# Kernel optimization log

Measured on AMD Instinct MI355X. Metric: run time of the kernel, lower is better.

The kernel has to match this reference:

```python
import jax, jax.numpy as jnp
import numpy as np
from jax import lax

N_IMG = 2
LEVEL_HW = [(200, 200), (100, 100), (50, 50), (25, 25), (13, 13)]
STRIDES = [4, 8, 16, 32, 64]
SIZES = [32.0, 64.0, 128.0, 256.0, 512.0]
A = 3
LEVEL_SIZES = [A * h * w for h, w in LEVEL_HW]
R = sum(LEVEL_SIZES)  # 159882
PRE_NMS = 1000   # pre_nms_top_n['testing']
POST_NMS = 1000  # post_nms_top_n['testing']
NMS_THRESH = 0.7
SCORE_THRESH = 0.0
MIN_SIZE = 1e-3
IMG_H = IMG_W = 800.0
BBOX_XFORM_CLIP = float(np.log(1000.0 / 16.0))


def _make_anchors():
    ratios = np.array([0.5, 1.0, 2.0])
    h_r = np.sqrt(ratios)
    w_r = 1.0 / h_r
    out = []
    for (h, w), stride, size in zip(LEVEL_HW, STRIDES, SIZES):
        ws = size * w_r
        hs = size * h_r
        base = np.stack([-ws / 2, -hs / 2, ws / 2, hs / 2], 1)  # [A,4]
        sx = (np.arange(w) + 0.5) * stride
        sy = (np.arange(h) + 0.5) * stride
        yy, xx = np.meshgrid(sy, sx, indexing='ij')
        shifts = np.stack([xx.ravel(), yy.ravel(), xx.ravel(), yy.ravel()], 1)  # [H*W,4]
        out.append((shifts[:, None, :] + base[None, :, :]).reshape(-1, 4))
    return np.concatenate(out, 0).astype(np.float32)  # [R,4]


def setup_inputs() -> dict:
    key = jax.random.key(0)
    k1, k2 = jax.random.split(key)
    objectness = jax.random.normal(k1, (N_IMG, R), jnp.float32)
    deltas = jax.random.normal(k2, (N_IMG, R, 4), jnp.float32) * 0.2
    anchors = jnp.asarray(_make_anchors())
    return {"objectness": objectness, "deltas": deltas, "anchors": anchors}


def _decode(deltas, anchors):
    # BoxCoder.decode with weights (1,1,1,1)
    wa = anchors[:, 2] - anchors[:, 0]
    ha = anchors[:, 3] - anchors[:, 1]
    cxa = anchors[:, 0] + 0.5 * wa
    cya = anchors[:, 1] + 0.5 * ha
    dx, dy, dw, dh = deltas[..., 0], deltas[..., 1], deltas[..., 2], deltas[..., 3]
    dw = jnp.minimum(dw, BBOX_XFORM_CLIP)
    dh = jnp.minimum(dh, BBOX_XFORM_CLIP)
    cx = dx * wa + cxa
    cy = dy * ha + cya
    w = jnp.exp(dw) * wa
    h = jnp.exp(dh) * ha
    return jnp.stack([cx - 0.5 * w, cy - 0.5 * h, cx + 0.5 * w, cy + 0.5 * h], -1)


def _nms_single(boxes, scores, lvl, valid):
    # batched_nms via per-level coordinate offset trick
    offs = lvl.astype(boxes.dtype) * (max(IMG_H, IMG_W) + 1.0)
    ob = boxes + offs[:, None]
    s = jnp.where(valid, scores, -1.0)
    order = jnp.argsort(-s)
    b = ob[order]          # offset boxes, score-descending
    raw = boxes[order]     # original boxes
    v = valid[order]
    ss = s[order]
    area = (b[:, 2] - b[:, 0]) * (b[:, 3] - b[:, 1])
    lt = jnp.maximum(b[:, None, :2], b[None, :, :2])
    rb = jnp.minimum(b[:, None, 2:], b[None, :, 2:])
    wh = jnp.clip(rb - lt, 0.0)
    inter = wh[..., 0] * wh[..., 1]
    iou = inter / (area[:, None] + area[None, :] - inter + 1e-9)  # [K,K]
    K = b.shape[0]

    def body(keep, i):
        suppressed = jnp.any(keep & (iou[:, i] > NMS_THRESH))
        keep = keep.at[i].set(v[i] & ~suppressed)
        return keep, None

    keep, _ = lax.scan(body, jnp.zeros((K,), bool), jnp.arange(K))
    # compact kept boxes (score order preserved) into fixed POST_NMS slots
    pos = jnp.where(keep, jnp.minimum(jnp.cumsum(keep) - 1, POST_NMS), POST_NMS)
    out_b = jnp.zeros((POST_NMS + 1, 4), boxes.dtype).at[pos].set(raw)[:POST_NMS]
    out_s = jnp.full((POST_NMS + 1,), -1.0, boxes.dtype).at[pos].set(ss)[:POST_NMS]
    return out_b, out_s


def _forward(objectness, deltas, anchors):
    proposals = _decode(deltas, anchors)  # [N,R,4]
    # per-level topk (pre_nms_top_n)
    idxs = []
    off = 0
    for n in LEVEL_SIZES:
        k = min(PRE_NMS, n)
        _, ti = lax.top_k(objectness[:, off:off + n], k)
        idxs.append(ti + off)
        off += n
    top_idx = jnp.concatenate(idxs, 1)  # [N,K]
    obj = jnp.take_along_axis(objectness, top_idx, 1)
    boxes = jnp.take_along_axis(proposals, top_idx[..., None], 1)
    levels = jnp.concatenate([jnp.full((n,), i, jnp.int32) for i, n in enumerate(LEVEL_SIZES)])
    lvl = levels[top_idx]
    scores = jax.nn.sigmoid(obj)
    # clip_boxes_to_image
    x1 = jnp.clip(boxes[..., 0], 0.0, IMG_W)
    y1 = jnp.clip(boxes[..., 1], 0.0, IMG_H)
    x2 = jnp.clip(boxes[..., 2], 0.0, IMG_W)
    y2 = jnp.clip(boxes[..., 3], 0.0, IMG_H)
    boxes = jnp.stack([x1, y1, x2, y2], -1)
    # remove_small_boxes + score_thresh -> validity mask (fixed shapes)
    valid = (x2 - x1 >= MIN_SIZE) & (y2 - y1 >= MIN_SIZE) & (scores >= SCORE_THRESH)
    return jax.vmap(_nms_single)(boxes, scores, lvl, valid)


def reference(objectness, deltas, anchors):
    return _forward(objectness, deltas, anchors)
```

## Files before the change

kernel.cpp:

```cpp
#include <hip/hip_runtime.h>

typedef unsigned long long u64;
typedef unsigned int u32;

#define R_TOT 159882
#define POST 1000
#define IMG_SZ 800.0f
#define NMS_TH 0.7f
#define BBOX_CLIP 4.135166556742356f
#define LCAP 1024

__device__ __forceinline__ float fadd_(float a, float b){ return __fadd_rn(a,b); }
__device__ __forceinline__ float fsub_(float a, float b){ return __fsub_rn(a,b); }
__device__ __forceinline__ float fmul_(float a, float b){ return __fmul_rn(a,b); }

__device__ __forceinline__ int lvl_len(int l){ const int L[5]={120000,30000,7500,1875,507}; return L[l]; }
__device__ __forceinline__ int lvl_off(int l){ const int L[5]={0,120000,150000,157500,159375}; return L[l]; }
__device__ __forceinline__ int lvl_k(int l){ const int L[5]={1000,1000,1000,1000,507}; return L[l]; }

__device__ __forceinline__ u32 mono_(u32 u){ return (u & 0x80000000u) ? ~u : (u | 0x80000000u); }

__device__ __forceinline__ u64 readlane64(u64 v, int i){
  u32 lo = (u32)__builtin_amdgcn_readlane((int)(u32)v, i);
  u32 hi = (u32)__builtin_amdgcn_readlane((int)(u32)(v >> 32), i);
  return ((u64)hi << 32) | (u64)lo;
}

__global__ __launch_bounds__(512) void k_histcollect(const float* __restrict__ obj,
                                                     u64* mainS, u64* tieS,
                                                     int* cntS, int* cnt2S,
                                                     int* bstarG, int* remG){
  int g = blockIdx.x, sl = blockIdx.y;
  int img = g/5, lvl = g%5;
  int n = lvl_len(lvl), s0 = lvl_off(lvl), k = lvl_k(lvl);
  int tid = threadIdx.x, lane = tid & 63, wid = tid >> 6;
  __shared__ __align__(16) char arena[16384];
  __shared__ int wsum[8];
  __shared__ int sh_bs, sh_rem, lc, lc2;
  int* lh = (int*)arena;
  for (int i = tid; i < 4096; i += 512) lh[i] = 0;
  __syncthreads();
  const float* p = obj + img*R_TOT + s0;

  {
    int full = n >> 12;
    for (int it = 0; it < full; it++){
      int e0 = (it << 12) + tid;
      float v[8];
      #pragma unroll
      for (int q = 0; q < 8; q++) v[q] = p[e0 + (q << 9)];
      #pragma unroll
      for (int q = 0; q < 8; q++){
        u32 mu = mono_(__float_as_uint(v[q]));
        atomicAdd(&lh[(~mu) >> 20], 1);
      }
    }
    int e0 = (full << 12) + tid;
    float v[8];
    #pragma unroll
    for (int q = 0; q < 8; q++){ int e = e0 + (q << 9); v[q] = (e < n) ? p[e] : 0.0f; }
    #pragma unroll
    for (int q = 0; q < 8; q++){
      int e = e0 + (q << 9);
      if (e < n){
        u32 mu = mono_(__float_as_uint(v[q]));
        atomicAdd(&lh[(~mu) >> 20], 1);
      }
    }
  }
  __syncthreads();

  int h[8];
  #pragma unroll
  for (int q = 0; q < 8; q++) h[q] = lh[8*tid + q];
  int part = 0;
  #pragma unroll
  for (int q = 0; q < 8; q++) part += h[q];
  int x = part;
  for (int d = 1; d < 64; d <<= 1){ int y = __shfl_up(x, d); if (lane >= d) x += y; }
  if (lane == 63) wsum[wid] = x;
  __syncthreads();
  int add = 0;
  for (int w = 0; w < wid; w++) add += wsum[w];
  int incl = x + add, excl = incl - part;
  if (excl < k && k <= incl){
    int cum = excl;
    #pragma unroll
    for (int q = 0; q < 8; q++){
      if (cum + h[q] >= k){
        sh_bs = 8*tid + q; sh_rem = k - cum;
        if (sl == 0){ bstarG[g] = 8*tid + q; remG[g] = k - cum; }
        break;
      }
      cum += h[q];
    }
  }
  __syncthreads();
  int bs = sh_bs;

  u64* lmain = (u64*)arena;
  u64* lbuf2 = (u64*)(arena + 8192);
  if (tid == 0){ lc = 0; lc2 = 0; }
  __syncthreads();
  int lo = (int)((long long)n * sl / 16), hiS = (int)((long long)n * (sl+1) / 16);
  int len = hiS - lo;
  {
    int full = len >> 12;
    for (int it = 0; it < full; it++){
      int e0 = lo + (it << 12) + tid;
      float v[8];
      #pragma unroll
      for (int q = 0; q < 8; q++) v[q] = p[e0 + (q << 9)];
      #pragma unroll
      for (int q = 0; q < 8; q++){
        int e = e0 + (q << 9);
        u32 mu = mono_(__float_as_uint(v[q]));
        u64 key56 = (((u64)(~mu)) << 24) | (u32)(s0 + e);
        int bin = (int)(key56 >> 44);
        if (bin < bs){ int pos = atomicAdd(&lc, 1); lmain[pos] = key56; }
        else if (bin == bs){ int pos = atomicAdd(&lc2, 1); if (pos < 1024) lbuf2[pos] = key56; }
      }
    }
    int e0 = lo + (full << 12) + tid;
    float v[8];
    #pragma unroll
    for (int q = 0; q < 8; q++){ int e = e0 + (q << 9); v[q] = (e < hiS) ? p[e] : 0.0f; }
    #pragma unroll
    for (int q = 0; q < 8; q++){
      int e = e0 + (q << 9);
      if (e < hiS){
        u32 mu = mono_(__float_as_uint(v[q]));
        u64 key56 = (((u64)(~mu)) << 24) | (u32)(s0 + e);
        int bin = (int)(key56 >> 44);
        if (bin < bs){ int pos = atomicAdd(&lc, 1); lmain[pos] = key56; }
        else if (bin == bs){ int pos = atomicAdd(&lc2, 1); if (pos < 1024) lbuf2[pos] = key56; }
      }
    }
  }
  __syncthreads();
  int idx16 = g*16 + sl;
  if (tid == 0){ cntS[idx16] = lc; cnt2S[idx16] = lc2; }
  for (int i = tid; i < lc; i += 512) mainS[idx16*1024 + i] = lmain[i];
  int c2l = lc2 < 1024 ? lc2 : 1024;
  for (int i = tid; i < c2l; i += 512) tieS[idx16*1024 + i] = lbuf2[i];
}

__global__ __launch_bounds__(1024) void k_seldecode(const float* __restrict__ obj,
                                                    const float4* __restrict__ deltas,
                                                    const float4* __restrict__ anchors,
                                                    const u64* __restrict__ mainS,
                                                    const u64* __restrict__ tieS,
                                                    const int* __restrict__ cntS,
                                                    const int* __restrict__ cnt2S,
                                                    const int* __restrict__ remG,
                                                    const int* __restrict__ bstarG,
                                                    float4* boxL, float* scoreL,
                                                    float4* nbox, u64* okeyN, int* ncnt){
  int g = blockIdx.x, img = g/5, lvl = g%5;
  int s0 = lvl_off(lvl), n = lvl_len(lvl), k = lvl_k(lvl);
  const float* p = obj + img*R_TOT + s0;
  __shared__ u64 Lbuf[LCAP];
  __shared__ u64 mainL[1024];
  __shared__ float4 lbox[1024];
  __shared__ u64 lokey[1024];
  __shared__ unsigned char lval[1024];
  __shared__ int h16[16];
  __shared__ int scnt[16], tcnt[16];
  __shared__ int sbase[17], tbase[17];
  __shared__ int sh_sc, sh_rem;
  __shared__ u64 sh_thr;
  int tid = threadIdx.x, lane = tid & 63;
  if (tid < 16){ scnt[tid] = cntS[g*16 + tid]; tcnt[tid] = cnt2S[g*16 + tid]; }
  __syncthreads();
  if (tid == 0){
    int s = 0, t2 = 0;
    #pragma unroll
    for (int q = 0; q < 16; q++){ sbase[q] = s; s += scnt[q]; tbase[q] = t2; t2 += tcnt[q]; }
    sbase[16] = s; tbase[16] = t2;
  }
  __syncthreads();
  int nb = sbase[16];
  int c2 = tbase[16];
  int rem = remG[g];
  int bs = bstarG[g];
  {
    u64 vmain = ~0ull;
    if (tid < nb){
      int sl = 0;
      #pragma unroll
      for (int q = 1; q < 16; q++) sl += (tid >= sbase[q]) ? 1 : 0;
      vmain = mainS[(g*16 + sl)*1024 + (tid - sbase[sl])];
    }
    mainL[tid] = vmain;
  }
  if (tid == 0){ sh_sc = 0; sh_rem = rem; }
  int c2c = c2 < LCAP ? c2 : LCAP;
  for (int e = tid; e < c2c; e += 1024){
    int sl = 0;
    #pragma unroll
    for (int q = 1; q < 16; q++) sl += (e >= tbase[q]) ? 1 : 0;
    Lbuf[e] = tieS[(g*16 + sl)*1024 + (e - tbase[sl])];
  }
  __syncthreads();
  if (c2 <= LCAP){
    for (int e = tid; e < c2; e += 1024){
      u64 kk = Lbuf[e];
      int rk = 0;
      for (int q = 0; q < c2; q++) rk += (Lbuf[q] < kk) ? 1 : 0;
      if (rk < rem){ int p2 = atomicAdd(&sh_sc, 1); mainL[nb + p2] = kk; }
    }
  } else {
    if (tid == 0) sh_thr = ((u64)bs) << 44;
    __syncthreads();
    for (int shift = 40; shift >= 0; shift -= 4){
      if (tid < 16) h16[tid] = 0;
      __syncthreads();
      u64 pref = sh_thr;
      u64 himask = ~((1ull << (shift+4)) - 1ull);
      for (int e = tid; e < n; e += 1024){
        u32 mu = mono_(__float_as_uint(p[e]));
        u64 kk = (((u64)(~mu)) << 24) | (u32)(s0 + e);
        if ((kk & himask) == (pref & himask)) atomicAdd(&h16[(int)((kk >> shift) & 15)], 1);
      }
      __syncthreads();
      if (tid == 0){
        int r2 = sh_rem, cum = 0;
        for (int d = 0; d < 16; d++){
          int hb = h16[d];
          if (cum + hb >= r2){ sh_thr = pref | ((u64)d << shift); sh_rem = r2 - cum; break; }
          cum += hb;
        }
      }
      __syncthreads();
    }
    u64 thr = sh_thr;
    for (int e = tid; e < n; e += 1024){
      u32 mu = mono_(__float_as_uint(p[e]));
      u64 kk = (((u64)(~mu)) << 24) | (u32)(s0 + e);
      if ((int)(kk >> 44) == bs && kk <= thr){ int p2 = atomicAdd(&sh_sc, 1); mainL[nb + p2] = kk; }
    }
  }
  __syncthreads();
  for (int k2 = 2; k2 <= 1024; k2 <<= 1){
    for (int j = k2 >> 1; j > 0; j >>= 1){
      __syncthreads();
      int i = tid, ixj = i ^ j;
      if (ixj > i){
        u64 a = mainL[i], b = mainL[ixj];
        bool up = (i & k2) == 0;
        if ((a > b) == up){ mainL[i] = b; mainL[ixj] = a; }
      }
    }
  }
  __syncthreads();
  int r = tid, t = g*1024 + r;
  if (r < k){
    int idx = (int)(mainL[r] & 0xFFFFFFu);
    float4 a = anchors[idx];
    float4 d = deltas[img*R_TOT + idx];
    float o = obj[img*R_TOT + idx];
    float wa = fsub_(a.z, a.x), ha = fsub_(a.w, a.y);
    float cxa = fadd_(a.x, fmul_(0.5f, wa)), cya = fadd_(a.y, fmul_(0.5f, ha));
    float dw = fminf(d.z, BBOX_CLIP), dh = fminf(d.w, BBOX_CLIP);
    float cx = fadd_(fmul_(d.x, wa), cxa), cy = fadd_(fmul_(d.y, ha), cya);
    float w  = fmul_(expf(dw), wa),        h  = fmul_(expf(dh), ha);
    float x1 = fsub_(cx, fmul_(0.5f, w)), y1 = fsub_(cy, fmul_(0.5f, h));
    float x2 = fadd_(cx, fmul_(0.5f, w)), y2 = fadd_(cy, fmul_(0.5f, h));
    x1 = fminf(fmaxf(x1, 0.0f), IMG_SZ); y1 = fminf(fmaxf(y1, 0.0f), IMG_SZ);
    x2 = fminf(fmaxf(x2, 0.0f), IMG_SZ); y2 = fminf(fmaxf(y2, 0.0f), IMG_SZ);
    bool valid = (fsub_(x2, x1) >= 1e-3f) && (fsub_(y2, y1) >= 1e-3f);
    float e = expf(-o);
    float sig = __fdiv_rn(1.0f, fadd_(1.0f, e));
    float s = valid ? sig : -1.0f;
    u32 sb = __float_as_uint(s);
    u32 ms = (sb & 0x80000000u) ? ~sb : (sb | 0x80000000u);
    float4 b4 = make_float4(x1, y1, x2, y2);
    boxL[t] = b4;
    scoreL[t] = sig;
    lokey[r] = (((u64)(~ms)) << 32) | (u32)(lvl*1000 + r);
    lbox[r] = b4;
    lval[r] = valid ? 1 : 0;
  } else {
    lval[r] = 0;
  }
  __syncthreads();
  if (tid < 64){
    int cnt = 0;
    float off = (float)lvl * 801.0f;
    for (int base = 0; base < k; base += 64){
      int r2 = base + lane;
      bool v = (r2 < k) && lval[r2];
      float4 b = lbox[r2 < k ? r2 : 0];
      u64 mask = __ballot(v);
      int before = __popcll(mask & ((1ull << lane) - 1ull));
      if (v){
        int pos = cnt + before;
        nbox[g*1024 + pos] = make_float4(fadd_(b.x,off), fadd_(b.y,off), fadd_(b.z,off), fadd_(b.w,off));
        okeyN[g*1024 + pos] = lokey[r2];
      }
      cnt += __popcll(mask);
    }
    if (lane == 0) ncnt[g] = cnt;
  }
}

__global__ __launch_bounds__(64) void k_mask(const float4* __restrict__ nbox,
                                             const int* __restrict__ ncnt,
                                             u64* LTG2){
  int g = blockIdx.x, tr = blockIdx.y, tw = blockIdx.z;
  if (tw > tr) return;
  int m = ncnt[g];
  if (tr*64 >= m) return;
  __shared__ float4 shb[64];
  __shared__ float sharea[64];
  int lane = threadIdx.x;
  if (tw*64 + lane < m){
    float4 b = nbox[g*1024 + tw*64 + lane];
    shb[lane] = b;
    sharea[lane] = fmul_(fsub_(b.z,b.x), fsub_(b.w,b.y));
  }
  __syncthreads();
  int j = tr*64 + lane;
  if (j >= m) return;
  float4 a = nbox[g*1024 + j];
  float areaA = fmul_(fsub_(a.z,a.x), fsub_(a.w,a.y));
  int imax = m - tw*64; if (imax > 64) imax = 64;
  if (tw == tr){
    u64 bitsF = 0;
    for (int ii = lane+1; ii < imax; ii++){
      float4 b = shb[ii];
      float ltx = fmaxf(a.x, b.x), lty = fmaxf(a.y, b.y);
      float rbx = fminf(a.z, b.z), rby = fminf(a.w, b.w);
      float wx = fmaxf(fsub_(rbx, ltx), 0.0f), wy = fmaxf(fsub_(rby, lty), 0.0f);
      float inter = fmul_(wx, wy);
      float den = fadd_(fsub_(fadd_(areaA, sharea[ii]), inter), 1e-9f);
      if (__fdiv_rn(inter, den) > NMS_TH) bitsF |= (1ull << ii);
    }
    LTG2[((size_t)(g*1024 + j))*16 + 15] = bitsF;
  } else {
    u64 bits = 0;
    for (int ii = 0; ii < imax; ii++){
      float4 b = shb[ii];
      float ltx = fmaxf(a.x, b.x), lty = fmaxf(a.y, b.y);
      float rbx = fminf(a.z, b.z), rby = fminf(a.w, b.w);
      float wx = fmaxf(fsub_(rbx, ltx), 0.0f), wy = fmaxf(fsub_(rby, lty), 0.0f);
      float inter = fmul_(wx, wy);
      float den = fadd_(fsub_(fadd_(areaA, sharea[ii]), inter), 1e-9f);
      if (__fdiv_rn(inter, den) > NMS_TH) bits |= (1ull << ii);
    }
    LTG2[((size_t)(g*1024 + j))*16 + tw] = bits;
  }
}

struct ChunkBuf {
  ulonglong2 v0, v1, v2, v3, v4, v5, v6, v7;
  u64 ok;
};

__device__ __forceinline__ void issue_chunk(const u64* __restrict__ LT2,
                                            const u64* __restrict__ oK,
                                            int c, int lane, ChunkBuf& b){
  int row = c*64 + lane;
  const ulonglong2* rp = (const ulonglong2*)(LT2 + (size_t)row*16);
  b.v0 = rp[0]; b.v1 = rp[1]; b.v2 = rp[2]; b.v3 = rp[3];
  b.v4 = rp[4]; b.v5 = rp[5]; b.v6 = rp[6]; b.v7 = rp[7];
  b.ok = oK[row];
}

__device__ __forceinline__ void consume_chunk(const ChunkBuf& b, int c, int m, int lane,
                                              u64* KwR, u64* runsL, int& cnt){
  int row = c*64 + lane;
  bool inr = row < m;
  u64 supp = 0;
  #define TERM(q, val) supp |= (((q) < c) ? (val) : 0ull) & KwR[q];
  TERM(0,  b.v0.x) TERM(1,  b.v0.y) TERM(2,  b.v1.x) TERM(3,  b.v1.y)
  TERM(4,  b.v2.x) TERM(5,  b.v2.y) TERM(6,  b.v3.x) TERM(7,  b.v3.y)
  TERM(8,  b.v4.x) TERM(9,  b.v4.y) TERM(10, b.v5.x) TERM(11, b.v5.y)
  TERM(12, b.v6.x) TERM(13, b.v6.y) TERM(14, b.v7.x)
  #undef TERM
  u64 fwd = inr ? b.v7.y : 0;
  u64 live = __ballot(inr && (supp == 0));
  u64 fz = __ballot(fwd != 0);
  u64 kept = 0;
  while (1){
    u64 lf = live & fz;
    if (!lf){ kept |= live; break; }
    int i = __builtin_ctzll(lf);
    u64 bi = 1ull << i;
    u64 below = live & (bi - 1ull);
    kept |= below | bi;
    live &= ~(below | bi);
    live &= ~readlane64(fwd, i);
  }
  KwR[c] = kept;
  bool kp = (kept >> lane) & 1ull;
  int before = __popcll(kept & ((1ull << lane) - 1ull));
  if (kp) runsL[cnt + before] = b.ok;
  cnt += __popcll(kept);
}

__global__ __launch_bounds__(1024) void k_scanmerge(const u64* __restrict__ LTG2,
                                                    const int* __restrict__ ncnt,
                                                    const u64* __restrict__ okeyN,
                                                    const float4* __restrict__ boxL,
                                                    const float* __restrict__ scoreL,
                                                    float* out){
  int img = blockIdx.x, tid = threadIdx.x, lane = tid & 63, wid = tid >> 6;
  __shared__ u64 runs[5*1024];
  __shared__ u64 Kw[5][16];
  __shared__ int cl[5];
  if (wid < 5){
    int l = wid, g = img*5 + l;
    int m = ncnt[g];
    int nch = (m + 63) >> 6;
    const u64* LT2 = LTG2 + ((size_t)g*1024)*16;
    const u64* oK = okeyN + g*1024;
    u64* KwR = &Kw[l][0];
    u64* runsL = &runs[l*1024];
    int cnt = 0;
    ChunkBuf A, B;
    if (nch > 0){
      issue_chunk(LT2, oK, 0, lane, A);
      int c = 0;
      while (c < nch){
        if (c+1 < nch) issue_chunk(LT2, oK, c+1, lane, B);
        consume_chunk(A, c, m, lane, KwR, runsL, cnt);
        c++;
        if (c >= nch) break;
        if (c+1 < nch) issue_chunk(LT2, oK, c+1, lane, A);
        consume_chunk(B, c, m, lane, KwR, runsL, cnt);
        c++;
      }
    }
    if (lane == 0) cl[l] = cnt;
  } else {
    for (int t = tid - 320; t < POST; t += 704){
      out[img*POST*4 + t*4 + 0] = 0.0f;
      out[img*POST*4 + t*4 + 1] = 0.0f;
      out[img*POST*4 + t*4 + 2] = 0.0f;
      out[img*POST*4 + t*4 + 3] = 0.0f;
      out[2*POST*4 + img*POST + t] = -1.0f;
    }
  }
  __syncthreads();
  for (int idx = tid; idx < 5*1024; idx += 1024){
    int l = idx >> 10, i = idx & 1023;
    if (i < cl[l]){
      u64 key = runs[l*1024 + i];
      int o0 = l+1; if (o0 >= 5) o0 -= 5;
      int o1 = l+2; if (o1 >= 5) o1 -= 5;
      int o2 = l+3; if (o2 >= 5) o2 -= 5;
      int o3 = l+4; if (o3 >= 5) o3 -= 5;
      const u64* r0 = runs + (o0 << 10);
      const u64* r1 = runs + (o1 << 10);
      const u64* r2 = runs + (o2 << 10);
      const u64* r3 = runs + (o3 << 10);
      int lo0 = 0, hi0 = cl[o0];
      int lo1 = 0, hi1 = cl[o1];
      int lo2 = 0, hi2 = cl[o2];
      int lo3 = 0, hi3 = cl[o3];
      #pragma unroll 1
      for (int st = 0; st < 11; st++){
        int m0 = (lo0+hi0)>>1, m1 = (lo1+hi1)>>1, m2 = (lo2+hi2)>>1, m3 = (lo3+hi3)>>1;
        u64 a0 = r0[m0], a1 = r1[m1], a2 = r2[m2], a3 = r3[m3];
        if (lo0 < hi0){ if (a0 < key) lo0 = m0+1; else hi0 = m0; }
        if (lo1 < hi1){ if (a1 < key) lo1 = m1+1; else hi1 = m1; }
        if (lo2 < hi2){ if (a2 < key) lo2 = m2+1; else hi2 = m2; }
        if (lo3 < hi3){ if (a3 < key) lo3 = m3+1; else hi3 = m3; }
      }
      int rank = i + lo0 + lo1 + lo2 + lo3;
      if (rank < POST){
        int pos = (int)(key & 0xFFFFFFFFull);
        int lvl = pos / 1000, r = pos - lvl*1000;
        int gg = img*5 + lvl;
        float4 bo = boxL[gg*1024 + r];
        float sc = scoreL[gg*1024 + r];
        out[img*POST*4 + rank*4 + 0] = bo.x;
        out[img*POST*4 + rank*4 + 1] = bo.y;
        out[img*POST*4 + rank*4 + 2] = bo.z;
        out[img*POST*4 + rank*4 + 3] = bo.w;
        out[2*POST*4 + img*POST + rank] = sc;
      }
    }
  }
}

extern "C" void kernel_launch(void* const* d_in, const int* in_sizes, int n_in,
                              void* d_out, int out_size, void* d_ws, size_t ws_size,
                              hipStream_t stream){
  (void)in_sizes; (void)n_in; (void)out_size; (void)ws_size;
  const float*  obj     = (const float*)d_in[0];
  const float4* deltas  = (const float4*)d_in[1];
  const float4* anchors = (const float4*)d_in[2];
  float* out = (float*)d_out;
  char* ws = (char*)d_ws;
  u64* mainS   = (u64*)(ws + 0);
  u64* tieS    = (u64*)(ws + 1310720);
  int* cntS    = (int*)(ws + 2621440);
  int* cnt2S   = (int*)(ws + 2622080);
  int* bstarG  = (int*)(ws + 2622720);
  int* remG    = (int*)(ws + 2622784);
  float4* boxL = (float4*)(ws + 2622848);
  float* scoreL= (float*)(ws + 2786688);
  u64* okeyN   = (u64*)(ws + 2827648);
  float4* nbox = (float4*)(ws + 2909568);
  u64* LTG2    = (u64*)(ws + 3073408);
  int* ncnt    = (int*)(ws + 4384128);

  {
    dim3 gh(10, 16);
    k_histcollect<<<gh, 512, 0, stream>>>(obj, mainS, tieS, cntS, cnt2S, bstarG, remG);
  }
  k_seldecode<<<10, 1024, 0, stream>>>(obj, deltas, anchors, mainS, tieS, cntS, cnt2S,
                                       remG, bstarG, boxL, scoreL, nbox, okeyN, ncnt);
  {
    dim3 gm(10, 16, 16);
    k_mask<<<gm, 64, 0, stream>>>(nbox, ncnt, LTG2);
  }
  k_scanmerge<<<2, 1024, 0, stream>>>(LTG2, ncnt, okeyN, boxL, scoreL, out);
}
```

Baseline: 150.8 us.

## Fuse histogram-collect and select-decode kernels using in-kernel spin-wait on slice flags

Merges the histogram/collect kernel and the per-level select/decode kernel into one launch. The last slice block of each group spins on per-slice magic flags written by the other fifteen slice blocks, then does the selection, bitonic sort and decode with 512 threads instead of 1024. This removes one kernel launch and its inter-kernel gap, at the cost of atomic global traffic and spin waiting. The flag protocol is never reset between calls, so a leftover MAGIC from a previous run could let the waiting block read stale data, and it relies on all blocks being co-resident.

```diff
diff --git a/kernel.cpp b/kernel.cpp
--- a/kernel.cpp
+++ b/kernel.cpp
@@ -9,6 +9,7 @@
 #define NMS_TH 0.7f
 #define BBOX_CLIP 4.135166556742356f
 #define LCAP 1024
+#define MAGIC 0x1B7E3A9Fu
 
 __device__ __forceinline__ float fadd_(float a, float b){ return __fadd_rn(a,b); }
 __device__ __forceinline__ float fsub_(float a, float b){ return __fsub_rn(a,b); }
@@ -26,17 +27,23 @@
   return ((u64)hi << 32) | (u64)lo;
 }
 
-__global__ __launch_bounds__(512) void k_histcollect(const float* __restrict__ obj,
-                                                     u64* mainS, u64* tieS,
-                                                     int* cntS, int* cnt2S,
-                                                     int* bstarG, int* remG){
+__global__ __launch_bounds__(512) void k_front(const float* __restrict__ obj,
+                                               const float4* __restrict__ deltas,
+                                               const float4* __restrict__ anchors,
+                                               u64* mainS, u64* tieS,
+                                               int* cntS, int* cnt2S, u32* mark,
+                                               float4* boxL, float* scoreL,
+                                               float4* nbox, u64* okeyN, int* ncnt){
   int g = blockIdx.x, sl = blockIdx.y;
   int img = g/5, lvl = g%5;
   int n = lvl_len(lvl), s0 = lvl_off(lvl), k = lvl_k(lvl);
   int tid = threadIdx.x, lane = tid & 63, wid = tid >> 6;
-  __shared__ __align__(16) char arena[16384];
+  __shared__ __align__(16) char arena[41984];
   __shared__ int wsum[8];
-  __shared__ int sh_bs, sh_rem, lc, lc2;
+  __shared__ int h16s[16];
+  __shared__ int scnt_[16], tcnt_[16], sbase[17], tbase[17];
+  __shared__ int sh_bs, sh_rem, lc, lc2, s_sc, s_rem2;
+  __shared__ u64 s_thr;
   int* lh = (int*)arena;
   for (int i = tid; i < 4096; i += 512) lh[i] = 0;
   __syncthreads();
@@ -87,11 +94,7 @@
     int cum = excl;
     #pragma unroll
     for (int q = 0; q < 8; q++){
-      if (cum + h[q] >= k){
-        sh_bs = 8*tid + q; sh_rem = k - cum;
-        if (sl == 0){ bstarG[g] = 8*tid + q; remG[g] = k - cum; }
-        break;
-      }
+      if (cum + h[q] >= k){ sh_bs = 8*tid + q; sh_rem = k - cum; break; }
       cum += h[q];
     }
   }
@@ -139,149 +142,143 @@
   }
   __syncthreads();
   int idx16 = g*16 + sl;
-  if (tid == 0){ cntS[idx16] = lc; cnt2S[idx16] = lc2; }
-  for (int i = tid; i < lc; i += 512) mainS[idx16*1024 + i] = lmain[i];
+  for (int i = tid; i < lc; i += 512) atomicExch(&mainS[idx16*1024 + i], lmain[i]);
   int c2l = lc2 < 1024 ? lc2 : 1024;
-  for (int i = tid; i < c2l; i += 512) tieS[idx16*1024 + i] = lbuf2[i];
-}
-
-__global__ __launch_bounds__(1024) void k_seldecode(const float* __restrict__ obj,
-                                                    const float4* __restrict__ deltas,
-                                                    const float4* __restrict__ anchors,
-                                                    const u64* __restrict__ mainS,
-                                                    const u64* __restrict__ tieS,
-                                                    const int* __restrict__ cntS,
-                                                    const int* __restrict__ cnt2S,
-                                                    const int* __restrict__ remG,
-                                                    const int* __restrict__ bstarG,
-                                                    float4* boxL, float* scoreL,
-                                                    float4* nbox, u64* okeyN, int* ncnt){
-  int g = blockIdx.x, img = g/5, lvl = g%5;
-  int s0 = lvl_off(lvl), n = lvl_len(lvl), k = lvl_k(lvl);
-  const float* p = obj + img*R_TOT + s0;
-  __shared__ u64 Lbuf[LCAP];
-  __shared__ u64 mainL[1024];
-  __shared__ float4 lbox[1024];
-  __shared__ u64 lokey[1024];
-  __shared__ unsigned char lval[1024];
-  __shared__ int h16[16];
-  __shared__ int scnt[16], tcnt[16];
-  __shared__ int sbase[17], tbase[17];
-  __shared__ int sh_sc, sh_rem;
-  __shared__ u64 sh_thr;
-  int tid = threadIdx.x, lane = tid & 63;
-  if (tid < 16){ scnt[tid] = cntS[g*16 + tid]; tcnt[tid] = cnt2S[g*16 + tid]; }
+  for (int i = tid; i < c2l; i += 512) atomicExch(&tieS[idx16*1024 + i], lbuf2[i]);
+  if (tid == 0){ atomicExch((u32*)&cntS[idx16], (u32)lc); atomicExch((u32*)&cnt2S[idx16], (u32)lc2); }
+  __threadfence();
+  __syncthreads();
+  if (sl != 15){
+    if (tid == 0) atomicExch(&mark[idx16], MAGIC);
+    return;
+  }
+  if (tid < 15){
+    while (atomicAdd(&mark[g*16 + tid], 0u) != MAGIC) __builtin_amdgcn_s_sleep(32);
+  }
+  __syncthreads();
+  __threadfence();
+
+  u64* mainL = (u64*)arena;
+  u64* Lbuf  = (u64*)(arena + 8192);
+  float4* lbox = (float4*)(arena + 16384);
+  u64* lokey = (u64*)(arena + 32768);
+  unsigned char* lval = (unsigned char*)(arena + 40960);
+  if (tid < 16){
+    scnt_[tid] = (int)atomicAdd((u32*)&cntS[g*16 + tid], 0u);
+    tcnt_[tid] = (int)atomicAdd((u32*)&cnt2S[g*16 + tid], 0u);
+  }
+  if (tid == 0){ s_sc = 0; s_rem2 = sh_rem; }
   __syncthreads();
   if (tid == 0){
     int s = 0, t2 = 0;
     #pragma unroll
-    for (int q = 0; q < 16; q++){ sbase[q] = s; s += scnt[q]; tbase[q] = t2; t2 += tcnt[q]; }
+    for (int q = 0; q < 16; q++){ sbase[q] = s; s += scnt_[q]; tbase[q] = t2; t2 += tcnt_[q]; }
     sbase[16] = s; tbase[16] = t2;
   }
   __syncthreads();
   int nb = sbase[16];
   int c2 = tbase[16];
-  int rem = remG[g];
-  int bs = bstarG[g];
-  {
-    u64 vmain = ~0ull;
-    if (tid < nb){
-      int sl = 0;
+  int rem = sh_rem;
+  for (int r = tid; r < 1024; r += 512){
+    u64 v = ~0ull;
+    if (r < nb){
+      int s = 0;
       #pragma unroll
-      for (int q = 1; q < 16; q++) sl += (tid >= sbase[q]) ? 1 : 0;
-      vmain = mainS[(g*16 + sl)*1024 + (tid - sbase[sl])];
-    }
-    mainL[tid] = vmain;
-  }
-  if (tid == 0){ sh_sc = 0; sh_rem = rem; }
+      for (int q = 1; q < 16; q++) s += (r >= sbase[q]) ? 1 : 0;
+      v = atomicAdd(&mainS[(g*16 + s)*1024 + (r - sbase[s])], 0ull);
+    }
+    mainL[r] = v;
+  }
   int c2c = c2 < LCAP ? c2 : LCAP;
-  for (int e = tid; e < c2c; e += 1024){
-    int sl = 0;
-    #pragma unroll
-    for (int q = 1; q < 16; q++) sl += (e >= tbase[q]) ? 1 : 0;
-    Lbuf[e] = tieS[(g*16 + sl)*1024 + (e - tbase[sl])];
+  for (int e = tid; e < c2c; e += 512){
+    int s = 0;
+    #pragma unroll
+    for (int q = 1; q < 16; q++) s += (e >= tbase[q]) ? 1 : 0;
+    Lbuf[e] = atomicAdd(&tieS[(g*16 + s)*1024 + (e - tbase[s])], 0ull);
   }
   __syncthreads();
   if (c2 <= LCAP){
-    for (int e = tid; e < c2; e += 1024){
+    for (int e = tid; e < c2; e += 512){
       u64 kk = Lbuf[e];
       int rk = 0;
       for (int q = 0; q < c2; q++) rk += (Lbuf[q] < kk) ? 1 : 0;
-      if (rk < rem){ int p2 = atomicAdd(&sh_sc, 1); mainL[nb + p2] = kk; }
+      if (rk < rem){ int p2 = atomicAdd(&s_sc, 1); mainL[nb + p2] = kk; }
     }
   } else {
-    if (tid == 0) sh_thr = ((u64)bs) << 44;
+    if (tid == 0) s_thr = ((u64)bs) << 44;
     __syncthreads();
     for (int shift = 40; shift >= 0; shift -= 4){
-      if (tid < 16) h16[tid] = 0;
+      if (tid < 16) h16s[tid] = 0;
       __syncthreads();
-      u64 pref = sh_thr;
+      u64 pref = s_thr;
       u64 himask = ~((1ull << (shift+4)) - 1ull);
-      for (int e = tid; e < n; e += 1024){
+      for (int e = tid; e < n; e += 512){
         u32 mu = mono_(__float_as_uint(p[e]));
         u64 kk = (((u64)(~mu)) << 24) | (u32)(s0 + e);
-        if ((kk & himask) == (pref & himask)) atomicAdd(&h16[(int)((kk >> shift) & 15)], 1);
+        if ((kk & himask) == (pref & himask)) atomicAdd(&h16s[(int)((kk >> shift) & 15)], 1);
       }
       __syncthreads();
       if (tid == 0){
-        int r2 = sh_rem, cum = 0;
+        int r2 = s_rem2, cum = 0;
         for (int d = 0; d < 16; d++){
-          int hb = h16[d];
-          if (cum + hb >= r2){ sh_thr = pref | ((u64)d << shift); sh_rem = r2 - cum; break; }
-          cum += hb;
+          int hb2 = h16s[d];
+          if (cum + hb2 >= r2){ s_thr = pref | ((u64)d << shift); s_rem2 = r2 - cum; break; }
+          cum += hb2;
         }
       }
       __syncthreads();
     }
-    u64 thr = sh_thr;
-    for (int e = tid; e < n; e += 1024){
+    u64 thr = s_thr;
+    for (int e = tid; e < n; e += 512){
       u32 mu = mono_(__float_as_uint(p[e]));
       u64 kk = (((u64)(~mu)) << 24) | (u32)(s0 + e);
-      if ((int)(kk >> 44) == bs && kk <= thr){ int p2 = atomicAdd(&sh_sc, 1); mainL[nb + p2] = kk; }
+      if ((int)(kk >> 44) == bs && kk <= thr){ int p2 = atomicAdd(&s_sc, 1); mainL[nb + p2] = kk; }
     }
   }
   __syncthreads();
   for (int k2 = 2; k2 <= 1024; k2 <<= 1){
     for (int j = k2 >> 1; j > 0; j >>= 1){
       __syncthreads();
-      int i = tid, ixj = i ^ j;
-      if (ixj > i){
-        u64 a = mainL[i], b = mainL[ixj];
-        bool up = (i & k2) == 0;
-        if ((a > b) == up){ mainL[i] = b; mainL[ixj] = a; }
-      }
-    }
-  }
-  __syncthreads();
-  int r = tid, t = g*1024 + r;
-  if (r < k){
-    int idx = (int)(mainL[r] & 0xFFFFFFu);
-    float4 a = anchors[idx];
-    float4 d = deltas[img*R_TOT + idx];
-    float o = obj[img*R_TOT + idx];
-    float wa = fsub_(a.z, a.x), ha = fsub_(a.w, a.y);
-    float cxa = fadd_(a.x, fmul_(0.5f, wa)), cya = fadd_(a.y, fmul_(0.5f, ha));
-    float dw = fminf(d.z, BBOX_CLIP), dh = fminf(d.w, BBOX_CLIP);
-    float cx = fadd_(fmul_(d.x, wa), cxa), cy = fadd_(fmul_(d.y, ha), cya);
-    float w  = fmul_(expf(dw), wa),        h  = fmul_(expf(dh), ha);
-    float x1 = fsub_(cx, fmul_(0.5f, w)), y1 = fsub_(cy, fmul_(0.5f, h));
-    float x2 = fadd_(cx, fmul_(0.5f, w)), y2 = fadd_(cy, fmul_(0.5f, h));
-    x1 = fminf(fmaxf(x1, 0.0f), IMG_SZ); y1 = fminf(fmaxf(y1, 0.0f), IMG_SZ);
-    x2 = fminf(fmaxf(x2, 0.0f), IMG_SZ); y2 = fminf(fmaxf(y2, 0.0f), IMG_SZ);
-    bool valid = (fsub_(x2, x1) >= 1e-3f) && (fsub_(y2, y1) >= 1e-3f);
-    float e = expf(-o);
-    float sig = __fdiv_rn(1.0f, fadd_(1.0f, e));
-    float s = valid ? sig : -1.0f;
-    u32 sb = __float_as_uint(s);
-    u32 ms = (sb & 0x80000000u) ? ~sb : (sb | 0x80000000u);
-    float4 b4 = make_float4(x1, y1, x2, y2);
-    boxL[t] = b4;
-    scoreL[t] = sig;
-    lokey[r] = (((u64)(~ms)) << 32) | (u32)(lvl*1000 + r);
-    lbox[r] = b4;
-    lval[r] = valid ? 1 : 0;
-  } else {
-    lval[r] = 0;
+      int i0 = tid;
+      int i = ((i0 & ~(j-1)) << 1) | (i0 & (j-1));
+      int ixj = i | j;
+      u64 a = mainL[i], b = mainL[ixj];
+      bool up = (i & k2) == 0;
+      if ((a > b) == up){ mainL[i] = b; mainL[ixj] = a; }
+    }
+  }
+  __syncthreads();
+  for (int r = tid; r < 1024; r += 512){
+    int t = g*1024 + r;
+    if (r < k){
+      int idx = (int)(mainL[r] & 0xFFFFFFu);
+      float4 a = anchors[idx];
+      float4 d = deltas[img*R_TOT + idx];
+      float o = obj[img*R_TOT + idx];
+      float wa = fsub_(a.z, a.x), ha = fsub_(a.w, a.y);
+      float cxa = fadd_(a.x, fmul_(0.5f, wa)), cya = fadd_(a.y, fmul_(0.5f, ha));
+      float dw = fminf(d.z, BBOX_CLIP), dh = fminf(d.w, BBOX_CLIP);
+      float cx = fadd_(fmul_(d.x, wa), cxa), cy = fadd_(fmul_(d.y, ha), cya);
+      float w  = fmul_(expf(dw), wa),        h2 = fmul_(expf(dh), ha);
+      float x1 = fsub_(cx, fmul_(0.5f, w)), y1 = fsub_(cy, fmul_(0.5f, h2));
+      float x2 = fadd_(cx, fmul_(0.5f, w)), y2 = fadd_(cy, fmul_(0.5f, h2));
+      x1 = fminf(fmaxf(x1, 0.0f), IMG_SZ); y1 = fminf(fmaxf(y1, 0.0f), IMG_SZ);
+      x2 = fminf(fmaxf(x2, 0.0f), IMG_SZ); y2 = fminf(fmaxf(y2, 0.0f), IMG_SZ);
+      bool valid = (fsub_(x2, x1) >= 1e-3f) && (fsub_(y2, y1) >= 1e-3f);
+      float e = expf(-o);
+      float sig = __fdiv_rn(1.0f, fadd_(1.0f, e));
+      float s = valid ? sig : -1.0f;
+      u32 sb = __float_as_uint(s);
+      u32 ms = (sb & 0x80000000u) ? ~sb : (sb | 0x80000000u);
+      float4 b4 = make_float4(x1, y1, x2, y2);
+      boxL[t] = b4;
+      scoreL[t] = sig;
+      lokey[r] = (((u64)(~ms)) << 32) | (u32)(lvl*1000 + r);
+      lbox[r] = b4;
+      lval[r] = valid ? 1 : 0;
+    } else {
+      lval[r] = 0;
+    }
   }
   __syncthreads();
   if (tid < 64){
@@ -498,21 +495,19 @@
   u64* tieS    = (u64*)(ws + 1310720);
   int* cntS    = (int*)(ws + 2621440);
   int* cnt2S   = (int*)(ws + 2622080);
-  int* bstarG  = (int*)(ws + 2622720);
-  int* remG    = (int*)(ws + 2622784);
-  float4* boxL = (float4*)(ws + 2622848);
-  float* scoreL= (float*)(ws + 2786688);
-  u64* okeyN   = (u64*)(ws + 2827648);
-  float4* nbox = (float4*)(ws + 2909568);
-  u64* LTG2    = (u64*)(ws + 3073408);
-  int* ncnt    = (int*)(ws + 4384128);
+  u32* mark    = (u32*)(ws + 2622720);
+  float4* boxL = (float4*)(ws + 2623360);
+  float* scoreL= (float*)(ws + 2787200);
+  u64* okeyN   = (u64*)(ws + 2828160);
+  float4* nbox = (float4*)(ws + 2910080);
+  u64* LTG2    = (u64*)(ws + 3073920);
+  int* ncnt    = (int*)(ws + 4384640);
 
   {
     dim3 gh(10, 16);
-    k_histcollect<<<gh, 512, 0, stream>>>(obj, mainS, tieS, cntS, cnt2S, bstarG, remG);
-  }
-  k_seldecode<<<10, 1024, 0, stream>>>(obj, deltas, anchors, mainS, tieS, cntS, cnt2S,
-                                       remG, bstarG, boxL, scoreL, nbox, okeyN, ncnt);
+    k_front<<<gh, 512, 0, stream>>>(obj, deltas, anchors, mainS, tieS, cntS, cnt2S, mark,
+                                    boxL, scoreL, nbox, okeyN, ncnt);
+  }
   {
     dim3 gm(10, 16, 16);
     k_mask<<<gm, 64, 0, stream>>>(nbox, ncnt, LTG2);
```

Result: slower. 176.1 us (+16.8%).
